# Kernel tuning notes

Hardware: AMD Instinct MI355X
Metric: run time of the kernel (lower is better)

The kernel has to match this reference:

```python
import jax, jax.numpy as jnp
import numpy as np

SINKHORN_ITERS = 20
SINKHORN_TEMP = 0.2


def log_sinkhorn(log_alpha, n_iters=SINKHORN_ITERS, temperature=SINKHORN_TEMP):
    """Log-domain Sinkhorn normalization over the last two dims."""
    log_alpha = log_alpha / temperature
    for _ in range(n_iters):
        log_alpha = log_alpha - jax.nn.logsumexp(log_alpha, axis=-1, keepdims=True)
        log_alpha = log_alpha - jax.nn.logsumexp(log_alpha, axis=-2, keepdims=True)
    return jnp.exp(log_alpha)


def setup_inputs() -> dict:
    key = jax.random.key(0)
    k_x, k_a, k_w1, k_wv = jax.random.split(key, 4)
    B = 64
    N, K, BASIS = 1024, 64, 8
    # xavier-uniform-like init scales
    a_bound = np.sqrt(6.0 / (N + N))
    w1_bound = np.sqrt(6.0 / (N + BASIS))
    wv_bound = np.sqrt(6.0 / (K + K))
    x = jax.random.normal(k_x, (B, N * K), dtype=jnp.float32)
    A_logits = jax.random.uniform(k_a, (N, N), dtype=jnp.float32, minval=-a_bound, maxval=a_bound)
    W_1 = jax.random.uniform(k_w1, (N, BASIS), dtype=jnp.float32, minval=-w1_bound, maxval=w1_bound)
    W_V = jax.random.uniform(k_wv, (BASIS, K, K), dtype=jnp.float32, minval=-wv_bound, maxval=wv_bound)
    return {"x": x, "A_logits": A_logits, "W_1": W_1, "W_V": W_V}


def reference(x, A_logits, W_1, W_V):
    B = x.shape[0]
    N, K = A_logits.shape[0], W_V.shape[-1]
    # Doubly-stochastic global mixing matrix A: [N, N]
    A = log_sinkhorn(A_logits)
    # Local block logits via basis combination: [N, K, K]
    W_logits = jnp.einsum('tk,kde->tde', W_1, W_V)
    W = log_sinkhorn(W_logits)
    x_reshaped = x.reshape(B, N, K)
    x_local = jnp.einsum('bni,nio->bno', x_reshaped, W)   # per-block KxK mix
    x_global = jnp.einsum('mn,bno->bmo', A, x_local)       # NxN block mix
    return x_global.reshape(B, N * K)
```

## Files before the change

kernel.cpp:

```cpp
#include <hip/hip_runtime.h>
#include <hip/hip_bf16.h>


#define N_DIM 1024
#define INV_T 5.0f
#define NBAR 16

typedef __attribute__((ext_vector_type(8))) short short8;
typedef __attribute__((ext_vector_type(4))) float float4v;

__device__ __forceinline__ float wave_red_sum(float x) {
#define DPP_ADD(C)                                                            \
  {                                                                           \
    int _y = __builtin_amdgcn_update_dpp(0, __float_as_int(x), (C), 0xf, 0xf, \
                                         true);                               \
    x += __int_as_float(_y);                                                  \
  }
  DPP_ADD(0x111);
  DPP_ADD(0x112);
  DPP_ADD(0x114);
  DPP_ADD(0x118);
  DPP_ADD(0x142);
  DPP_ADD(0x143);
#undef DPP_ADD
  return x;
}

__global__ __launch_bounds__(1024) void k_front(
    const float* __restrict__ x, const float* __restrict__ L,
    const float* __restrict__ W1, const float* __restrict__ WV,
    float* __restrict__ E0, __hip_bfloat16* __restrict__ Eh,
    __hip_bfloat16* __restrict__ El, float* __restrict__ P,
    unsigned* __restrict__ ctrl, float* __restrict__ u_g,
    float* __restrict__ v_g, float* __restrict__ XL, int write_bf16) {
  __shared__ __align__(16) float smem[9600];
  const int t = threadIdx.x;
  const int bid = blockIdx.x;
  const int lane = t & 63;
  const int w = t >> 6;

  if (bid < NBAR) {
    float* v_s = smem;
    float* uS = smem + 1024;
    float* red = smem + 1024 + 64;
    const int b = bid;
    const int r0 = b * 64;

    float e[4][16];
#pragma unroll
    for (int j = 0; j < 4; ++j) {
      const int r = r0 + 4 * w + j;
      const float* Lr = L + (size_t)r * N_DIM + lane;
#pragma unroll
      for (int k = 0; k < 16; ++k) e[j][k] = __expf(Lr[k * 64] * INV_T);
      if (write_bf16) {
        __hip_bfloat16* EhR = Eh + (size_t)r * N_DIM + lane;
        __hip_bfloat16* ElR = El + (size_t)r * N_DIM + lane;
#pragma unroll
        for (int k = 0; k < 16; ++k) {
          __hip_bfloat16 h = __float2bfloat16(e[j][k]);
          EhR[k * 64] = h;
          ElR[k * 64] = __float2bfloat16(e[j][k] - __bfloat162float(h));
        }
      } else {
        float* ER = E0 + (size_t)r * N_DIM + lane;
#pragma unroll
        for (int k = 0; k < 16; ++k) ER[k * 64] = e[j][k];
      }
    }
    v_s[t] = 1.0f;
    __syncthreads();

    for (int it = 0; it < 20; ++it) {
      float vv[16];
#pragma unroll
      for (int k = 0; k < 16; ++k) vv[k] = v_s[k * 64 + lane];
      float u[4];
#pragma unroll
      for (int j = 0; j < 4; ++j) {
        float p = 0.f;
#pragma unroll
        for (int k = 0; k < 16; ++k) p += e[j][k] * vv[k];
        p = wave_red_sum(p);
        u[j] = 1.0f /
               __int_as_float(__builtin_amdgcn_readlane(__float_as_int(p), 63));
      }
      float cpl[16];
#pragma unroll
      for (int k = 0; k < 16; ++k)
        cpl[k] = e[0][k] * u[0] + e[1][k] * u[1] + e[2][k] * u[2] +
                 e[3][k] * u[3];
      if (w >= 8) {
#pragma unroll
        for (int k = 0; k < 16; ++k)
          red[(w - 8) * 1028 + k * 64 + lane] = cpl[k];
      }
      __syncthreads();
      if (w < 8) {
#pragma unroll
        for (int k = 0; k < 16; ++k) red[w * 1028 + k * 64 + lane] += cpl[k];
      }
      __syncthreads();
      float cp = 0.f;
#pragma unroll
      for (int ww = 0; ww < 8; ++ww) cp += red[ww * 1028 + t];
      float* Pit = P + (size_t)it * (NBAR * N_DIM);
      __hip_atomic_store(&Pit[b * N_DIM + t], cp, __ATOMIC_RELAXED,
                         __HIP_MEMORY_SCOPE_AGENT);
      if (it == 19 && lane == 0) {
#pragma unroll
        for (int j = 0; j < 4; ++j) uS[4 * w + j] = u[j];
      }
      unsigned vals[NBAR];
#pragma unroll
      for (int pb = 0; pb < NBAR; ++pb)
        vals[pb] = (pb == b)
                       ? __float_as_uint(cp)
                       : __hip_atomic_load(
                             (const unsigned*)&Pit[pb * N_DIM + t],
                             __ATOMIC_RELAXED, __HIP_MEMORY_SCOPE_AGENT);
      for (;;) {
        unsigned miss = 0u;
#pragma unroll
        for (int pb = 0; pb < NBAR; ++pb) miss |= (vals[pb] == 0u) ? 1u : 0u;
        if (miss == 0u) break;
#pragma unroll
        for (int pb = 0; pb < NBAR; ++pb)
          if (vals[pb] == 0u)
            vals[pb] = __hip_atomic_load(
                (const unsigned*)&Pit[pb * N_DIM + t], __ATOMIC_RELAXED,
                __HIP_MEMORY_SCOPE_AGENT);
      }
      float s2 = 0.f;
#pragma unroll
      for (int pb = 0; pb < NBAR; ++pb) s2 += __uint_as_float(vals[pb]);
      v_s[t] = 1.0f / s2;
      __syncthreads();
    }
    if (t < 64) u_g[r0 + t] = uS[t];
    if (b == 0) v_g[t] = v_s[t];
    __syncthreads();
  }

  {
    float* uS2 = smem;
    float* ps = smem + 64;
    float* Ws = smem + 64 + 1024;
    float* Xs = smem + 64 + 1024 + 4096;
    unsigned* nsh = (unsigned*)(smem + 9500);
    unsigned* ticket = ctrl + 64;

    if (t == 0)
      nsh[0] = __hip_atomic_fetch_add(ticket, 1u, __ATOMIC_RELAXED,
                                      __HIP_MEMORY_SCOPE_AGENT);
    __syncthreads();
    int slot = 0;
    for (;;) {
      const unsigned n = nsh[slot];
      if (n >= 1024u) break;
      if (t == 0)
        nsh[slot ^ 1] = __hip_atomic_fetch_add(ticket, 1u, __ATOMIC_RELAXED,
                                               __HIP_MEMORY_SCOPE_AGENT);
      float w1[8];
#pragma unroll
      for (int k = 0; k < 8; ++k) w1[k] = W1[n * 8 + k];

      float ew[4];
#pragma unroll
      for (int j = 0; j < 4; ++j) {
        const int f = j * 1024 + t;
        float acc = 0.f;
#pragma unroll
        for (int k = 0; k < 8; ++k) acc += w1[k] * WV[k * 4096 + f];
        ew[j] = __expf(acc * INV_T);
      }

      float vt = 1.0f;
      for (int it = 0; it < 20; ++it) {
#pragma unroll
        for (int j = 0; j < 4; ++j) {
          float pp = wave_red_sum(ew[j] * vt);
          if (lane == 63) uS2[j * 16 + w] = 1.0f / pp;
        }
        float cp2 = 0.f;
#pragma unroll
        for (int j = 0; j < 4; ++j) cp2 += ew[j] * uS2[j * 16 + w];
        ps[w * 64 + lane] = cp2;
        __syncthreads();
        float sv = 0.f;
#pragma unroll
        for (int ww = 0; ww < 16; ++ww) sv += ps[ww * 64 + lane];
        vt = 1.0f / sv;
        __syncthreads();
      }

#pragma unroll
      for (int j = 0; j < 4; ++j)
        Ws[(j * 16 + w) * 64 + lane] = ew[j] * uS2[j * 16 + w] * vt;
#pragma unroll
      for (int j = 0; j < 4; ++j) {
        const int f = j * 1024 + t;
        Xs[(f >> 6) * 65 + (f & 63)] =
            x[(size_t)(f >> 6) * 65536 + n * 64 + (f & 63)];
      }
      __syncthreads();

      const int bb = t >> 4;
      const int o4 = (t & 15) * 4;
      float4 a4 = {0.f, 0.f, 0.f, 0.f};
#pragma unroll 4
      for (int i = 0; i < 64; ++i) {
        float4 w4 = *(const float4*)&Ws[i * 64 + o4];
        float xv = Xs[bb * 65 + i];
        a4.x += xv * w4.x;
        a4.y += xv * w4.y;
        a4.z += xv * w4.z;
        a4.w += xv * w4.w;
      }
      *(float4*)&XL[(size_t)n * 4096 + bb * 64 + o4] = a4;
      __syncthreads();
      slot ^= 1;
    }
  }
}

__global__ __launch_bounds__(256) void k_xt(const float* __restrict__ XL,
                                            const float* __restrict__ v_g,
                                            __hip_bfloat16* __restrict__ XTh,
                                            __hip_bfloat16* __restrict__ XTl) {
  __shared__ float T[64 * 68];
  __shared__ float vsh[64];
  const int t = threadIdx.x;
  const int n0 = blockIdx.x * 64;
  const int c0 = blockIdx.y * 64;
  if (t < 64) vsh[t] = v_g[n0 + t];
  {
    const int r = t >> 4;
    const int c4 = (t & 15) * 4;
#pragma unroll
    for (int p = 0; p < 4; ++p) {
      float4 f =
          *(const float4*)&XL[(size_t)(n0 + r + 16 * p) * 4096 + c0 + c4];
      *(float4*)&T[(r + 16 * p) * 68 + c4] = f;
    }
  }
  __syncthreads();
  const int cl = t >> 2;
  const int nb = (t & 3) * 16;
  __align__(16) __hip_bfloat16 hbuf[16];
  __align__(16) __hip_bfloat16 lbuf[16];
#pragma unroll
  for (int j = 0; j < 16; ++j) {
    float xv = T[(nb + j) * 68 + cl] * vsh[nb + j];
    __hip_bfloat16 h = __float2bfloat16(xv);
    hbuf[j] = h;
    lbuf[j] = __float2bfloat16(xv - __bfloat162float(h));
  }
  const size_t off = (size_t)(c0 + cl) * 1024 + n0 + nb;
  *(uint4*)&XTh[off] = *(uint4*)&hbuf[0];
  *(uint4*)&XTh[off + 8] = *(uint4*)&hbuf[8];
  *(uint4*)&XTl[off] = *(uint4*)&lbuf[0];
  *(uint4*)&XTl[off + 8] = *(uint4*)&lbuf[8];
}

#define LSTR 72
__global__ __launch_bounds__(256) void k_gemm3(
    const ushort* __restrict__ Eh, const ushort* __restrict__ El,
    const ushort* __restrict__ XTh, const ushort* __restrict__ XTl,
    const float* __restrict__ u_g, float* __restrict__ out) {
  __shared__ ushort As[128 * LSTR];
  __shared__ ushort Xs[128 * LSTR];
  __shared__ float ush[128];
  const int t = threadIdx.x;
  const int m0 = blockIdx.x * 128;
  const int c0 = blockIdx.y * 128;
  const int wid = t >> 6, lane = t & 63;
  const int wm = (wid & 1) * 64, wc = (wid >> 1) * 64;
  const int lm = lane & 15, q = lane >> 4;
  const int sr = t >> 1;
  const int sc = (t & 1) * 32;
  if (t < 128) ush[t] = u_g[m0 + t];

  float4v acc[4][4];
#pragma unroll
  for (int i = 0; i < 4; ++i)
#pragma unroll
    for (int j = 0; j < 4; ++j) acc[i][j] = (float4v){0.f, 0.f, 0.f, 0.f};

  for (int seg = 0; seg < 3; ++seg) {
    const ushort* Ag = (seg == 1) ? El : Eh;
    const ushort* Xg = (seg == 2) ? XTl : XTh;
    for (int k0 = 0; k0 < 1024; k0 += 64) {
      __syncthreads();
      const ushort* ag = Ag + (size_t)(m0 + sr) * 1024 + k0 + sc;
      const ushort* xg = Xg + (size_t)(c0 + sr) * 1024 + k0 + sc;
      uint4 a0 = *(const uint4*)(ag);
      uint4 a1 = *(const uint4*)(ag + 8);
      uint4 a2 = *(const uint4*)(ag + 16);
      uint4 a3 = *(const uint4*)(ag + 24);
      uint4 x0 = *(const uint4*)(xg);
      uint4 x1 = *(const uint4*)(xg + 8);
      uint4 x2 = *(const uint4*)(xg + 16);
      uint4 x3 = *(const uint4*)(xg + 24);
      *(uint4*)&As[sr * LSTR + sc] = a0;
      *(uint4*)&As[sr * LSTR + sc + 8] = a1;
      *(uint4*)&As[sr * LSTR + sc + 16] = a2;
      *(uint4*)&As[sr * LSTR + sc + 24] = a3;
      *(uint4*)&Xs[sr * LSTR + sc] = x0;
      *(uint4*)&Xs[sr * LSTR + sc + 8] = x1;
      *(uint4*)&Xs[sr * LSTR + sc + 16] = x2;
      *(uint4*)&Xs[sr * LSTR + sc + 24] = x3;
      __syncthreads();
#pragma unroll
      for (int kk = 0; kk < 2; ++kk) {
        short8 af[4], xf[4];
#pragma unroll
        for (int i = 0; i < 4; ++i)
          af[i] = *(const short8*)&As[(wm + 16 * i + lm) * LSTR + kk * 32 +
                                      q * 8];
#pragma unroll
        for (int j = 0; j < 4; ++j)
          xf[j] = *(const short8*)&Xs[(wc + 16 * j + lm) * LSTR + kk * 32 +
                                      q * 8];
#pragma unroll
        for (int i = 0; i < 4; ++i)
#pragma unroll
          for (int j = 0; j < 4; ++j)
            acc[i][j] = __builtin_amdgcn_mfma_f32_16x16x32_bf16(
                af[i], xf[j], acc[i][j], 0, 0, 0);
      }
    }
  }
#pragma unroll
  for (int i = 0; i < 4; ++i) {
#pragma unroll
    for (int j = 0; j < 4; ++j) {
      const int ml = wm + 16 * i + q * 4;
      const int m = m0 + ml;
      const int c = c0 + wc + 16 * j + lm;
      const int bb = c >> 6, o = c & 63;
      float* dst = out + (size_t)bb * 65536 + (size_t)m * 64 + o;
#pragma unroll
      for (int r = 0; r < 4; ++r) dst[64 * r] = acc[i][j][r] * ush[ml + r];
    }
  }
}

__global__ __launch_bounds__(256) void k_gemm(const float* __restrict__ E0,
                                              const float* __restrict__ XL,
                                              const float* __restrict__ u_g,
                                              const float* __restrict__ v_g,
                                              float* __restrict__ out) {
  __shared__ float Asm[32][132];
  __shared__ float Xsm[32][132];
  const int t = threadIdx.x;
  const int m0 = blockIdx.x * 128;
  const int c0 = blockIdx.y * 128;
  const int my8 = (t >> 4) * 8;
  const int cx8 = (t & 15) * 8;
  const int kk = t & 31;
  const int rr = t >> 5;
  float acc[8][8] = {};

  for (int k0 = 0; k0 < 1024; k0 += 32) {
#pragma unroll
    for (int s = 0; s < 16; ++s)
      Asm[kk][rr + 8 * s] = E0[(size_t)(m0 + rr + 8 * s) * 1024 + k0 + kk];
#pragma unroll
    for (int s = 0; s < 4; ++s) {
      const int krow = k0 + rr + 8 * s;
      float vk = v_g[krow];
      float4 f = *(const float4*)&XL[(size_t)krow * 4096 + c0 + kk * 4];
      f.x *= vk;
      f.y *= vk;
      f.z *= vk;
      f.w *= vk;
      *(float4*)&Xsm[rr + 8 * s][kk * 4] = f;
    }
    __syncthreads();
#pragma unroll
    for (int k = 0; k < 32; ++k) {
      float a[8], xv[8];
      *(float4*)&a[0] = *(const float4*)&Asm[k][my8];
      *(float4*)&a[4] = *(const float4*)&Asm[k][my8 + 4];
      *(float4*)&xv[0] = *(const float4*)&Xsm[k][cx8];
      *(float4*)&xv[4] = *(const float4*)&Xsm[k][cx8 + 4];
#pragma unroll
      for (int i = 0; i < 8; ++i)
#pragma unroll
        for (int j = 0; j < 8; ++j) acc[i][j] += a[i] * xv[j];
    }
    __syncthreads();
  }

#pragma unroll
  for (int i = 0; i < 8; ++i) {
    const int m = m0 + my8 + i;
    const float um = u_g[m];
    const int c = c0 + cx8;
    const int bb = c >> 6, o = c & 63;
    float* dst = out + (size_t)bb * 65536 + (size_t)m * 64 + o;
#pragma unroll
    for (int j = 0; j < 8; ++j) dst[j] = acc[i][j] * um;
  }
}

extern "C" void kernel_launch(void* const* d_in, const int* in_sizes, int n_in,
                              void* d_out, int out_size, void* d_ws,
                              size_t ws_size, hipStream_t stream) {
  (void)in_sizes;
  (void)n_in;
  (void)out_size;
  const float* x = (const float*)d_in[0];
  const float* Alog = (const float*)d_in[1];
  const float* W1 = (const float*)d_in[2];
  const float* WV = (const float*)d_in[3];
  float* out = (float*)d_out;

  char* ws = (char*)d_ws;
  const size_t MB = 1024 * 1024;
  const size_t KB = 1024;
  const bool use_bf16 = ws_size >= (40 * MB + 256 * KB);
  const size_t P_BYTES = 20ull * NBAR * N_DIM * sizeof(float);

  float* E0;
  float* XL;
  float* P;
  float* u_g;
  float* v_g;
  unsigned* ctrl;
  __hip_bfloat16 *Eh = nullptr, *El = nullptr, *XTh = nullptr, *XTl = nullptr;
  if (use_bf16) {
    P = (float*)(ws);
    E0 = (float*)(ws);
    XL = (float*)(ws + 4 * MB);
    Eh = (__hip_bfloat16*)(ws + 20 * MB);
    El = (__hip_bfloat16*)(ws + 22 * MB);
    XTh = (__hip_bfloat16*)(ws + 24 * MB);
    XTl = (__hip_bfloat16*)(ws + 32 * MB);
    u_g = (float*)(ws + 40 * MB);
    v_g = (float*)(ws + 40 * MB + 4 * KB);
    ctrl = (unsigned*)(ws + 40 * MB + 8 * KB);
  } else {
    E0 = (float*)(ws);
    XL = (float*)(ws + 4 * MB);
    P = (float*)(ws + 20 * MB);
    u_g = (float*)(ws + 20 * MB + 1536 * KB);
    v_g = (float*)(ws + 20 * MB + 1540 * KB);
    ctrl = (unsigned*)(ws + 20 * MB + 1544 * KB);
  }

  hipMemsetAsync(ctrl, 0, 4096, stream);
  hipMemsetAsync(P, 0, P_BYTES, stream);
  hipLaunchKernelGGL(k_front, dim3(256), dim3(1024), 0, stream, x, Alog, W1,
                     WV, E0, Eh, El, P, ctrl, u_g, v_g, XL, use_bf16 ? 1 : 0);
  if (use_bf16) {
    hipLaunchKernelGGL(k_xt, dim3(16, 64), dim3(256), 0, stream, XL, v_g, XTh,
                       XTl);
    hipLaunchKernelGGL(k_gemm3, dim3(8, 32), dim3(256), 0, stream,
                       (const ushort*)Eh, (const ushort*)El, (const ushort*)XTh,
                       (const ushort*)XTl, u_g, out);
  } else {
    hipLaunchKernelGGL(k_gemm, dim3(8, 32), dim3(256), 0, stream, E0, XL, u_g,
                       v_g, out);
  }
}
```

Baseline: 282.1 us.

## Process two local Sinkhorn blocks per ticket and spread A-Sinkhorn blocks across XCDs

Each work ticket in the front kernel now handles a pair of blocks. The two Sinkhorn iterations are interleaved, so they share the WV loads, the wave reductions and the per-iteration barriers, which halves the barrier count per block. The A-matrix Sinkhorn role moves from block IDs 0..15 to every eighth block ID, spreading these blocks across the chiplets (XCDs) rather than concentrating them. The cost is more registers and LDS per block, and coarser ticket granularity, which may reduce load balance.

After: 287.8 us. +2.0%, slower.

```diff
diff --git a/kernel.cpp b/kernel.cpp
--- a/kernel.cpp
+++ b/kernel.cpp
@@ -33,17 +33,19 @@
     __hip_bfloat16* __restrict__ El, float* __restrict__ P,
     unsigned* __restrict__ ctrl, float* __restrict__ u_g,
     float* __restrict__ v_g, float* __restrict__ XL, int write_bf16) {
-  __shared__ __align__(16) float smem[9600];
+  __shared__ __align__(16) float smem[10440];
   const int t = threadIdx.x;
   const int bid = blockIdx.x;
   const int lane = t & 63;
   const int w = t >> 6;
 
-  if (bid < NBAR) {
+  const bool is_a = ((bid & 7) == 0) && (bid < 8 * NBAR);
+
+  if (is_a) {
     float* v_s = smem;
     float* uS = smem + 1024;
     float* red = smem + 1024 + 64;
-    const int b = bid;
+    const int b = bid >> 3;
     const int r0 = b * 64;
 
     float e[4][16];
@@ -138,16 +140,18 @@
       __syncthreads();
     }
     if (t < 64) u_g[r0 + t] = uS[t];
-    if (b == 0) v_g[t] = v_s[t];
+    if (bid == 0) v_g[t] = v_s[t];
     __syncthreads();
   }
 
   {
-    float* uS2 = smem;
-    float* ps = smem + 64;
-    float* Ws = smem + 64 + 1024;
-    float* Xs = smem + 64 + 1024 + 4096;
-    unsigned* nsh = (unsigned*)(smem + 9500);
+    float* uSa = smem;
+    float* uSb = smem + 64;
+    float* psA = smem + 128;
+    float* psB = smem + 1152;
+    float* Ws = smem + 2176;
+    float* Xs = smem + 6272;
+    unsigned* nsh = (unsigned*)(smem + 10432);
     unsigned* ticket = ctrl + 64;
 
     if (t == 0)
@@ -156,68 +160,117 @@
     __syncthreads();
     int slot = 0;
     for (;;) {
-      const unsigned n = nsh[slot];
-      if (n >= 1024u) break;
+      const unsigned pr = nsh[slot];
+      if (pr >= 512u) break;
       if (t == 0)
         nsh[slot ^ 1] = __hip_atomic_fetch_add(ticket, 1u, __ATOMIC_RELAXED,
                                                __HIP_MEMORY_SCOPE_AGENT);
-      float w1[8];
-#pragma unroll
-      for (int k = 0; k < 8; ++k) w1[k] = W1[n * 8 + k];
-
-      float ew[4];
+      const int na = (int)(pr * 2u);
+      const int nb = na + 1;
+      float w1a[8], w1b[8];
+#pragma unroll
+      for (int k = 0; k < 8; ++k) w1a[k] = W1[na * 8 + k];
+#pragma unroll
+      for (int k = 0; k < 8; ++k) w1b[k] = W1[nb * 8 + k];
+
+      float ewa[4], ewb[4];
 #pragma unroll
       for (int j = 0; j < 4; ++j) {
         const int f = j * 1024 + t;
-        float acc = 0.f;
-#pragma unroll
-        for (int k = 0; k < 8; ++k) acc += w1[k] * WV[k * 4096 + f];
-        ew[j] = __expf(acc * INV_T);
-      }
-
-      float vt = 1.0f;
+        float aa = 0.f, ab = 0.f;
+#pragma unroll
+        for (int k = 0; k < 8; ++k) {
+          const float wv = WV[k * 4096 + f];
+          aa += w1a[k] * wv;
+          ab += w1b[k] * wv;
+        }
+        ewa[j] = __expf(aa * INV_T);
+        ewb[j] = __expf(ab * INV_T);
+      }
+
+      float vta = 1.0f, vtb = 1.0f;
       for (int it = 0; it < 20; ++it) {
 #pragma unroll
         for (int j = 0; j < 4; ++j) {
-          float pp = wave_red_sum(ew[j] * vt);
-          if (lane == 63) uS2[j * 16 + w] = 1.0f / pp;
-        }
-        float cp2 = 0.f;
-#pragma unroll
-        for (int j = 0; j < 4; ++j) cp2 += ew[j] * uS2[j * 16 + w];
-        ps[w * 64 + lane] = cp2;
+          float pa = wave_red_sum(ewa[j] * vta);
+          float pb = wave_red_sum(ewb[j] * vtb);
+          if (lane == 63) {
+            uSa[j * 16 + w] = 1.0f / pa;
+            uSb[j * 16 + w] = 1.0f / pb;
+          }
+        }
+        float cpa = 0.f, cpb = 0.f;
+#pragma unroll
+        for (int j = 0; j < 4; ++j) {
+          cpa += ewa[j] * uSa[j * 16 + w];
+          cpb += ewb[j] * uSb[j * 16 + w];
+        }
+        psA[w * 64 + lane] = cpa;
+        psB[w * 64 + lane] = cpb;
         __syncthreads();
-        float sv = 0.f;
-#pragma unroll
-        for (int ww = 0; ww < 16; ++ww) sv += ps[ww * 64 + lane];
-        vt = 1.0f / sv;
+        float sva = 0.f, svb = 0.f;
+#pragma unroll
+        for (int ww = 0; ww < 16; ++ww) {
+          sva += psA[ww * 64 + lane];
+          svb += psB[ww * 64 + lane];
+        }
+        vta = 1.0f / sva;
+        vtb = 1.0f / svb;
         __syncthreads();
       }
 
 #pragma unroll
       for (int j = 0; j < 4; ++j)
-        Ws[(j * 16 + w) * 64 + lane] = ew[j] * uS2[j * 16 + w] * vt;
+        Ws[(j * 16 + w) * 64 + lane] = ewa[j] * uSa[j * 16 + w] * vta;
 #pragma unroll
       for (int j = 0; j < 4; ++j) {
         const int f = j * 1024 + t;
         Xs[(f >> 6) * 65 + (f & 63)] =
-            x[(size_t)(f >> 6) * 65536 + n * 64 + (f & 63)];
-      }
-      __syncthreads();
-
-      const int bb = t >> 4;
-      const int o4 = (t & 15) * 4;
-      float4 a4 = {0.f, 0.f, 0.f, 0.f};
+            x[(size_t)(f >> 6) * 65536 + na * 64 + (f & 63)];
+      }
+      __syncthreads();
+      {
+        const int bb = t >> 4;
+        const int o4 = (t & 15) * 4;
+        float4 a4 = {0.f, 0.f, 0.f, 0.f};
 #pragma unroll 4
-      for (int i = 0; i < 64; ++i) {
-        float4 w4 = *(const float4*)&Ws[i * 64 + o4];
-        float xv = Xs[bb * 65 + i];
-        a4.x += xv * w4.x;
-        a4.y += xv * w4.y;
-        a4.z += xv * w4.z;
-        a4.w += xv * w4.w;
-      }
-      *(float4*)&XL[(size_t)n * 4096 + bb * 64 + o4] = a4;
+        for (int i = 0; i < 64; ++i) {
+          float4 w4 = *(const float4*)&Ws[i * 64 + o4];
+          float xv = Xs[bb * 65 + i];
+          a4.x += xv * w4.x;
+          a4.y += xv * w4.y;
+          a4.z += xv * w4.z;
+          a4.w += xv * w4.w;
+        }
+        *(float4*)&XL[(size_t)na * 4096 + bb * 64 + o4] = a4;
+      }
+      __syncthreads();
+
+#pragma unroll
+      for (int j = 0; j < 4; ++j)
+        Ws[(j * 16 + w) * 64 + lane] = ewb[j] * uSb[j * 16 + w] * vtb;
+#pragma unroll
+      for (int j = 0; j < 4; ++j) {
+        const int f = j * 1024 + t;
+        Xs[(f >> 6) * 65 + (f & 63)] =
+            x[(size_t)(f >> 6) * 65536 + nb * 64 + (f & 63)];
+      }
+      __syncthreads();
+      {
+        const int bb = t >> 4;
+        const int o4 = (t & 15) * 4;
+        float4 a4 = {0.f, 0.f, 0.f, 0.f};
+#pragma unroll 4
+        for (int i = 0; i < 64; ++i) {
+          float4 w4 = *(const float4*)&Ws[i * 64 + o4];
+          float xv = Xs[bb * 65 + i];
+          a4.x += xv * w4.x;
+          a4.y += xv * w4.y;
+          a4.z += xv * w4.z;
+          a4.w += xv * w4.w;
+        }
+        *(float4*)&XL[(size_t)nb * 4096 + bb * 64 + o4] = a4;
+      }
       __syncthreads();
       slot ^= 1;
     }
```

## Run per-block Sinkhorn in one wavefront with a register butterfly reduction

Applied to the files above, without the earlier changes.

Each 64x64 local block's Sinkhorn is now handled by a single wavefront that keeps the whole block in registers. Row sums use a ds_bpermute butterfly transpose-reduce, so the per-iteration block-wide __syncthreads and LDS partial sums go away. The dynamic atomic ticket scheduler is replaced by a static assignment of blocks to wavefronts, which also drops the ctrl memset, and x is read straight from global memory for the local mix. In exchange, each wave needs about 64+32 floats of registers, only 4 of the 16 wavefronts per workgroup do work, and the static split can leave the load unbalanced.

Result: slower. 1.063 ms (+276.9%).

```diff
diff --git a/kernel.cpp b/kernel.cpp
--- a/kernel.cpp
+++ b/kernel.cpp
@@ -33,11 +33,12 @@
     __hip_bfloat16* __restrict__ El, float* __restrict__ P,
     unsigned* __restrict__ ctrl, float* __restrict__ u_g,
     float* __restrict__ v_g, float* __restrict__ XL, int write_bf16) {
-  __shared__ __align__(16) float smem[9600];
+  __shared__ __align__(16) float smem[9312];
   const int t = threadIdx.x;
   const int bid = blockIdx.x;
   const int lane = t & 63;
   const int w = t >> 6;
+  (void)ctrl;
 
   if (bid < NBAR) {
     float* v_s = smem;
@@ -139,87 +140,105 @@
     }
     if (t < 64) u_g[r0 + t] = uS[t];
     if (b == 0) v_g[t] = v_s[t];
-    __syncthreads();
-  }
-
-  {
-    float* uS2 = smem;
-    float* ps = smem + 64;
-    float* Ws = smem + 64 + 1024;
-    float* Xs = smem + 64 + 1024 + 4096;
-    unsigned* nsh = (unsigned*)(smem + 9500);
-    unsigned* ticket = ctrl + 64;
-
-    if (t == 0)
-      nsh[0] = __hip_atomic_fetch_add(ticket, 1u, __ATOMIC_RELAXED,
-                                      __HIP_MEMORY_SCOPE_AGENT);
-    __syncthreads();
-    int slot = 0;
-    for (;;) {
-      const unsigned n = nsh[slot];
-      if (n >= 1024u) break;
-      if (t == 0)
-        nsh[slot ^ 1] = __hip_atomic_fetch_add(ticket, 1u, __ATOMIC_RELAXED,
-                                               __HIP_MEMORY_SCOPE_AGENT);
-      float w1[8];
-#pragma unroll
-      for (int k = 0; k < 8; ++k) w1[k] = W1[n * 8 + k];
-
-      float ew[4];
-#pragma unroll
-      for (int j = 0; j < 4; ++j) {
-        const int f = j * 1024 + t;
-        float acc = 0.f;
-#pragma unroll
-        for (int k = 0; k < 8; ++k) acc += w1[k] * WV[k * 4096 + f];
-        ew[j] = __expf(acc * INV_T);
-      }
-
-      float vt = 1.0f;
-      for (int it = 0; it < 20; ++it) {
-#pragma unroll
-        for (int j = 0; j < 4; ++j) {
-          float pp = wave_red_sum(ew[j] * vt);
-          if (lane == 63) uS2[j * 16 + w] = 1.0f / pp;
+    return;
+  }
+
+  if (w >= 4) return;
+  float* ug = smem + w * 64;
+
+  int nlist[2];
+  int rounds;
+  if (bid < 32) {
+    rounds = 2;
+    nlist[0] = (bid - 16) * 8 + w;
+    nlist[1] = (bid - 16) * 8 + 4 + w;
+  } else {
+    rounds = 1;
+    nlist[0] = 128 + (bid - 32) * 4 + w;
+    nlist[1] = 0;
+  }
+
+  const int pidx = lane << 2;
+
+  for (int r = 0; r < rounds; ++r) {
+    const int n = nlist[r];
+    float w1[8];
+#pragma unroll
+    for (int k = 0; k < 8; ++k) w1[k] = W1[n * 8 + k];
+    float e[64];
+#pragma unroll
+    for (int i = 0; i < 64; ++i) {
+      float acc = 0.f;
+#pragma unroll
+      for (int k = 0; k < 8; ++k) acc += w1[k] * WV[k * 4096 + i * 64 + lane];
+      e[i] = __expf(acc * INV_T);
+    }
+
+    float v = 1.0f;
+    for (int it = 0; it < 20; ++it) {
+      float a[32];
+      {
+        const bool hi = (lane & 32) != 0;
+        const int pj = pidx ^ (32 << 2);
+#pragma unroll
+        for (int j = 0; j < 32; ++j) {
+          float s0 = (hi ? e[j] : e[j + 32]) * v;
+          float k0 = (hi ? e[j + 32] : e[j]) * v;
+          a[j] = k0 + __int_as_float(__builtin_amdgcn_ds_bpermute(
+                          pj, __float_as_int(s0)));
         }
-        float cp2 = 0.f;
-#pragma unroll
-        for (int j = 0; j < 4; ++j) cp2 += ew[j] * uS2[j * 16 + w];
-        ps[w * 64 + lane] = cp2;
-        __syncthreads();
-        float sv = 0.f;
-#pragma unroll
-        for (int ww = 0; ww < 16; ++ww) sv += ps[ww * 64 + lane];
-        vt = 1.0f / sv;
-        __syncthreads();
-      }
-
-#pragma unroll
-      for (int j = 0; j < 4; ++j)
-        Ws[(j * 16 + w) * 64 + lane] = ew[j] * uS2[j * 16 + w] * vt;
-#pragma unroll
-      for (int j = 0; j < 4; ++j) {
-        const int f = j * 1024 + t;
-        Xs[(f >> 6) * 65 + (f & 63)] =
-            x[(size_t)(f >> 6) * 65536 + n * 64 + (f & 63)];
-      }
-      __syncthreads();
-
-      const int bb = t >> 4;
-      const int o4 = (t & 15) * 4;
-      float4 a4 = {0.f, 0.f, 0.f, 0.f};
+      }
+#define BSTAGE(D)                                                          \
+  {                                                                        \
+    const bool hi = (lane & (D)) != 0;                                     \
+    const int pj = pidx ^ ((D) << 2);                                      \
+    _Pragma("unroll") for (int j = 0; j < (D); ++j) {                      \
+      float s0 = hi ? a[j] : a[j + (D)];                                   \
+      float k0 = hi ? a[j + (D)] : a[j];                                   \
+      a[j] = k0 + __int_as_float(                                          \
+                      __builtin_amdgcn_ds_bpermute(pj, __float_as_int(s0))); \
+    }                                                                      \
+  }
+      BSTAGE(16)
+      BSTAGE(8)
+      BSTAGE(4)
+      BSTAGE(2)
+      BSTAGE(1)
+#undef BSTAGE
+      const float u_l = 1.0f / a[0];
+      ug[lane] = u_l;
+      float s2 = 0.f;
+#pragma unroll
+      for (int q = 0; q < 16; ++q) {
+        float4 u4 = *(const float4*)&ug[4 * q];
+        s2 += e[4 * q] * u4.x + e[4 * q + 1] * u4.y + e[4 * q + 2] * u4.z +
+              e[4 * q + 3] * u4.w;
+      }
+      v = 1.0f / s2;
+    }
+
+#pragma unroll
+    for (int q = 0; q < 16; ++q) {
+      float4 u4 = *(const float4*)&ug[4 * q];
+      e[4 * q] *= u4.x;
+      e[4 * q + 1] *= u4.y;
+      e[4 * q + 2] *= u4.z;
+      e[4 * q + 3] *= u4.w;
+    }
+
+    const float* xn = x + (size_t)n * 64;
+    float* xl = XL + (size_t)n * 4096;
 #pragma unroll 4
-      for (int i = 0; i < 64; ++i) {
-        float4 w4 = *(const float4*)&Ws[i * 64 + o4];
-        float xv = Xs[bb * 65 + i];
-        a4.x += xv * w4.x;
-        a4.y += xv * w4.y;
-        a4.z += xv * w4.z;
-        a4.w += xv * w4.w;
-      }
-      *(float4*)&XL[(size_t)n * 4096 + bb * 64 + o4] = a4;
-      __syncthreads();
-      slot ^= 1;
+    for (int bb = 0; bb < 64; ++bb) {
+      const float* xr = xn + (size_t)bb * 65536;
+      float acc = 0.f;
+#pragma unroll
+      for (int q = 0; q < 16; ++q) {
+        float4 xb = *(const float4*)&xr[4 * q];
+        acc += xb.x * e[4 * q] + xb.y * e[4 * q + 1] + xb.z * e[4 * q + 2] +
+               xb.w * e[4 * q + 3];
+      }
+      xl[bb * 64 + lane] = acc * v;
     }
   }
 }
@@ -450,7 +469,6 @@
     ctrl = (unsigned*)(ws + 20 * MB + 1544 * KB);
   }
 
-  hipMemsetAsync(ctrl, 0, 4096, stream);
   hipMemsetAsync(P, 0, P_BYTES, stream);
   hipLaunchKernelGGL(k_front, dim3(256), dim3(1024), 0, stream, x, Alog, W1,
                      WV, E0, Eh, El, P, ctrl, u_g, v_g, XL, use_bf16 ? 1 : 0);
```
